# Performance work log

Measured on AMD Instinct MI355X. Metric: run time of the kernel, lower is better.

## Reference

```python
import jax, jax.numpy as jnp
import numpy as np

B, T, C = 4, 2048, 1024   # batch, seq_len, n_embd
H, D = 16, 64             # num heads, head dim (H*D == C)


def setup_inputs() -> dict:
    key = jax.random.key(0)
    ks = jax.random.split(key, 6)
    scale = 0.02
    x = jax.random.normal(ks[0], (B, T, C), dtype=jnp.float32)
    Wq = jax.random.normal(ks[1], (H, C, D), dtype=jnp.float32) * scale
    Wk = jax.random.normal(ks[2], (H, C, D), dtype=jnp.float32) * scale
    Wv = jax.random.normal(ks[3], (H, C, D), dtype=jnp.float32) * scale
    Wp = jax.random.normal(ks[4], (C, C), dtype=jnp.float32) * scale
    bp = jnp.zeros((C,), dtype=jnp.float32)
    return {"x": x, "Wq": Wq, "Wk": Wk, "Wv": Wv, "Wp": Wp, "bp": bp}


def reference(x, Wq, Wk, Wv, Wp, bp):
    # Batched per-head projections (equivalent to the per-head nn.Linear loop)
    q = jnp.einsum('btc,hcd->bhtd', x, Wq)
    k = jnp.einsum('btc,hcd->bhtd', x, Wk)
    v = jnp.einsum('btc,hcd->bhtd', x, Wv)
    # NOTE: original code scales by C**-0.5 where C = n_embd (not head dim)
    scores = jnp.einsum('bhtd,bhsd->bhts', q, k) * (C ** -0.5)
    causal = jnp.tril(jnp.ones((T, T), dtype=bool))  # [T, T]
    scores = jnp.where(causal, scores, -jnp.inf)
    att = jax.nn.softmax(scores, axis=-1)            # [B, H, T, T]
    out = jnp.einsum('bhts,bhsd->bhtd', att, v)      # [B, H, T, D]
    # concat heads (order matches torch.cat over head list) then output proj
    out = out.transpose(0, 2, 1, 3).reshape(B, T, H * D)
    return out @ Wp + bp
```

## Files before the change

kernel.cpp:

```cpp
#include <hip/hip_runtime.h>
#include <hip/hip_bf16.h>


#define B_ 4
#define T_ 2048
#define C_ 1024
#define H_ 16
#define D_ 64
#define M_ (B_*T_)

typedef unsigned short u16;
typedef unsigned short ushort8 __attribute__((ext_vector_type(8)));
typedef unsigned int uint4v __attribute__((ext_vector_type(4)));
typedef int int2v __attribute__((ext_vector_type(2)));
typedef __attribute__((ext_vector_type(8))) short bf16x8;
typedef __attribute__((ext_vector_type(4))) float f32x4;
typedef __attribute__((ext_vector_type(16))) float f32x16;

__device__ __forceinline__ u16 f2bf(float f) {
    __hip_bfloat16 h = __float2bfloat16(f);
    return *reinterpret_cast<u16*>(&h);
}

__device__ __forceinline__ unsigned pkt(float lo, float hi2) {
    return __builtin_amdgcn_perm(__float_as_uint(hi2), __float_as_uint(lo), 0x07060302u);
}

__device__ __forceinline__ void gload_lds16(const void* g, void* lds) {
    __builtin_amdgcn_global_load_lds((const __attribute__((address_space(1))) unsigned int*)g,
                                     (__attribute__((address_space(3))) unsigned int*)lds, 16, 0, 0);
}

__global__ __launch_bounds__(256) void cast_x(const float* __restrict__ in, u16* __restrict__ out) {
    int i = (blockIdx.x * 256 + threadIdx.x) * 8;
    float4 a = *reinterpret_cast<const float4*>(in + i);
    float4 b = *reinterpret_cast<const float4*>(in + i + 4);
    ushort8 o;
    o[0]=f2bf(a.x); o[1]=f2bf(a.y); o[2]=f2bf(a.z); o[3]=f2bf(a.w);
    o[4]=f2bf(b.x); o[5]=f2bf(b.y); o[6]=f2bf(b.z); o[7]=f2bf(b.w);
    *reinterpret_cast<ushort8*>(out + i) = o;
}

__device__ __forceinline__ void ttile64(const float* __restrict__ in, int ldin,
                                        u16* __restrict__ out, int ldout, float scale) {
    __shared__ float t[64][65];
    const int tid = threadIdx.x;
    {
        int c = tid & 63, rr = tid >> 6;
        #pragma unroll
        for (int i = 0; i < 16; ++i) {
            int r = i * 4 + rr;
            t[r][c] = in[(size_t)r * ldin + c];
        }
    }
    __syncthreads();
    {
        int r2 = tid & 63, cg = tid >> 6;
        #pragma unroll
        for (int i = 0; i < 16; ++i) {
            int cc = i * 4 + cg;
            out[(size_t)cc * ldout + r2] = f2bf(t[r2][cc] * scale);
        }
    }
}

__global__ __launch_bounds__(256) void tw_qkv(const float* __restrict__ Wq, const float* __restrict__ Wk,
                                              const float* __restrict__ Wv, u16* __restrict__ Wt) {
    const int z = blockIdx.y;
    const int which = z >> 4, h = z & 15;
    const float* W = (which == 0 ? Wq : which == 1 ? Wk : Wv) + (size_t)h * C_ * D_;
    const int r0 = blockIdx.x * 64;
    const float scale = (which == 0) ? 0.03125f * 1.4426950408889634f : 1.f;
    ttile64(W + (size_t)r0 * D_, D_, Wt + (size_t)(which * 16 + h) * 64 * C_ + r0, C_, scale);
}

__global__ __launch_bounds__(256) void tw_p(const float* __restrict__ Wp, u16* __restrict__ Wpt) {
    const int r0 = blockIdx.x * 64, c0 = blockIdx.y * 64;
    ttile64(Wp + (size_t)r0 * C_ + c0, C_, Wpt + (size_t)c0 * C_ + r0, C_, 1.f);
}

__global__ __launch_bounds__(256) void tv(const u16* __restrict__ v, u16* __restrict__ vT) {
    __shared__ u16 t[64][72];
    const int tid = threadIdx.x;
    const int t0 = blockIdx.x * 64, bh = blockIdx.y;
    const u16* src = v + ((size_t)bh * T_ + t0) * D_;
    #pragma unroll
    for (int it = 0; it < 2; ++it) {
        int idx = it * 256 + tid;
        int r = idx >> 3, c8 = (idx & 7) * 8;
        *reinterpret_cast<ushort8*>(&t[r][c8]) =
            *reinterpret_cast<const ushort8*>(src + (size_t)r * D_ + c8);
    }
    __syncthreads();
    #pragma unroll
    for (int it = 0; it < 2; ++it) {
        int idx = it * 256 + tid;
        int d = idx >> 3, c8 = (idx & 7) * 8;
        ushort8 w;
        #pragma unroll
        for (int i = 0; i < 8; ++i) w[i] = t[c8 + i][d];
        *reinterpret_cast<ushort8*>(vT + ((size_t)bh * D_ + d) * T_ + t0 + c8) = w;
    }
}

__device__ __forceinline__ void gemm128_core(const u16* __restrict__ A, const u16* __restrict__ Bt,
                                             int m0, int n0, int K,
                                             u16* Asm, u16* Bsm, f32x4 (&acc)[4][4]) {
    const int tid = threadIdx.x;
    const int wid = tid >> 6, lane = tid & 63;
    const int l16 = lane & 15, lq = lane >> 4;
    const int wm = wid >> 1, wn = wid & 1;
    const int srow = lane >> 2;
    const int scol = (lane & 3) * 8;

    for (int k0 = 0; k0 < K; k0 += 32) {
        __syncthreads();
        #pragma unroll
        for (int it = 0; it < 2; ++it) {
            int row = wid * 32 + it * 16 + srow;
            gload_lds16(A  + (size_t)(m0 + row) * K + k0 + scol, Asm + wid * 1024 + it * 512);
            gload_lds16(Bt + (size_t)(n0 + row) * K + k0 + scol, Bsm + wid * 1024 + it * 512);
        }
        __syncthreads();
        bf16x8 af[4], bfr[4];
        #pragma unroll
        for (int t = 0; t < 4; ++t) {
            af[t]  = *reinterpret_cast<const bf16x8*>(Asm + (wm * 64 + t * 16 + l16) * 32 + lq * 8);
            bfr[t] = *reinterpret_cast<const bf16x8*>(Bsm + (wn * 64 + t * 16 + l16) * 32 + lq * 8);
        }
        #pragma unroll
        for (int mt = 0; mt < 4; ++mt)
            #pragma unroll
            for (int nt = 0; nt < 4; ++nt)
                acc[mt][nt] = __builtin_amdgcn_mfma_f32_16x16x32_bf16(af[mt], bfr[nt], acc[mt][nt], 0, 0, 0);
    }
}

__global__ __launch_bounds__(256) void qkv_gemm(const u16* __restrict__ xb, const u16* __restrict__ Wt,
                                                u16* __restrict__ q, u16* __restrict__ k, u16* __restrict__ v) {
    __shared__ u16 Asm[128 * 32], Bsm[128 * 32];
    f32x4 acc[4][4];
    #pragma unroll
    for (int i = 0; i < 4; ++i)
        #pragma unroll
        for (int j = 0; j < 4; ++j) { acc[i][j][0]=0.f; acc[i][j][1]=0.f; acc[i][j][2]=0.f; acc[i][j][3]=0.f; }
    const int m0 = blockIdx.x * 128, n0 = blockIdx.y * 128;
    gemm128_core(xb, Wt, m0, n0, C_, Asm, Bsm, acc);

    const int tid = threadIdx.x, wid = tid >> 6, lane = tid & 63;
    const int l16 = lane & 15, lq = lane >> 4;
    const int wm = wid >> 1, wn = wid & 1;
    #pragma unroll
    for (int mt = 0; mt < 4; ++mt) {
        #pragma unroll
        for (int j = 0; j < 4; ++j) {
            int m = m0 + wm * 64 + mt * 16 + lq * 4 + j;
            int b = m >> 11, t = m & (T_ - 1);
            #pragma unroll
            for (int nt = 0; nt < 4; ++nt) {
                int n = n0 + wn * 64 + nt * 16 + l16;
                int which = n >> 10, h = (n >> 6) & 15, d = n & 63;
                u16* dst = (which == 0 ? q : which == 1 ? k : v);
                dst[((size_t)(b * H_ + h) * T_ + t) * D_ + d] = f2bf(acc[mt][nt][j]);
            }
        }
    }
}

__global__ __launch_bounds__(256) void out_gemm(const u16* __restrict__ ob, const u16* __restrict__ Wpt,
                                                const float* __restrict__ bp, float* __restrict__ out) {
    __shared__ u16 Asm[128 * 32], Bsm[128 * 32];
    f32x4 acc[4][4];
    #pragma unroll
    for (int i = 0; i < 4; ++i)
        #pragma unroll
        for (int j = 0; j < 4; ++j) { acc[i][j][0]=0.f; acc[i][j][1]=0.f; acc[i][j][2]=0.f; acc[i][j][3]=0.f; }
    const int m0 = blockIdx.x * 128, n0 = blockIdx.y * 128;
    gemm128_core(ob, Wpt, m0, n0, C_, Asm, Bsm, acc);

    const int tid = threadIdx.x, wid = tid >> 6, lane = tid & 63;
    const int l16 = lane & 15, lq = lane >> 4;
    const int wm = wid >> 1, wn = wid & 1;
    #pragma unroll
    for (int mt = 0; mt < 4; ++mt) {
        #pragma unroll
        for (int j = 0; j < 4; ++j) {
            int m = m0 + wm * 64 + mt * 16 + lq * 4 + j;
            #pragma unroll
            for (int nt = 0; nt < 4; ++nt) {
                int n = n0 + wn * 64 + nt * 16 + l16;
                out[(size_t)m * C_ + n] = acc[mt][nt][j] + bp[n];
            }
        }
    }
}

template<int CUR>
__device__ __forceinline__ void attn_tile(const char* const (&pf)[4], const bf16x8 (&qf)[4],
                                          const f32x16& z16, float& lrun,
                                          f32x16& oacc0, f32x16& oacc1,
                                          bool isdiag, int relq, int hi) {
    f32x16 st0, st1;
    __builtin_amdgcn_s_setprio(1);
    {
        bf16x8 ka0 = *reinterpret_cast<const bf16x8*>(pf[0] + CUR * 8192);
        bf16x8 ka1 = *reinterpret_cast<const bf16x8*>(pf[0] + CUR * 8192 + 4096);
        st0 = __builtin_amdgcn_mfma_f32_32x32x16_bf16(ka0, qf[0], z16, 0, 0, 0);
        st1 = __builtin_amdgcn_mfma_f32_32x32x16_bf16(ka1, qf[0], z16, 0, 0, 0);
    }
    #pragma unroll
    for (int kc = 1; kc < 4; ++kc) {
        bf16x8 ka0 = *reinterpret_cast<const bf16x8*>(pf[kc] + CUR * 8192);
        bf16x8 ka1 = *reinterpret_cast<const bf16x8*>(pf[kc] + CUR * 8192 + 4096);
        st0 = __builtin_amdgcn_mfma_f32_32x32x16_bf16(ka0, qf[kc], st0, 0, 0, 0);
        st1 = __builtin_amdgcn_mfma_f32_32x32x16_bf16(ka1, qf[kc], st1, 0, 0, 0);
    }
    __builtin_amdgcn_s_setprio(0);

    if (isdiag) {
        #pragma unroll
        for (int rr = 0; rr < 16; ++rr) {
            int sl = (rr & 3) + 8 * (rr >> 2) + 4 * hi;
            if (sl > relq)      st0[rr] = -INFINITY;
            if (sl + 32 > relq) st1[rr] = -INFINITY;
        }
    }

    float rsum = 0.f;
    #pragma unroll
    for (int rr = 0; rr < 16; ++rr) {
        st0[rr] = __builtin_amdgcn_exp2f(st0[rr]);
        st1[rr] = __builtin_amdgcn_exp2f(st1[rr]);
        rsum += st0[rr] + st1[rr];
    }
    rsum += __shfl_xor(rsum, 32);
    lrun += rsum;

    bf16x8 pa0, pa1, pa2, pa3;
#if __has_builtin(__builtin_amdgcn_permlane32_swap)
#define MK_PA(PA, SV, RB)                                                          \
    {                                                                              \
        int X0 = (int)pkt(SV[RB + 0], SV[RB + 1]);                                 \
        int X1 = (int)pkt(SV[RB + 2], SV[RB + 3]);                                 \
        int Y0 = (int)pkt(SV[RB + 4], SV[RB + 5]);                                 \
        int Y1 = (int)pkt(SV[RB + 6], SV[RB + 7]);                                 \
        int2v r0 = __builtin_amdgcn_permlane32_swap(X0, Y0, false, false);         \
        int2v r1 = __builtin_amdgcn_permlane32_swap(X1, Y1, false, false);         \
        uint4v w; w[0] = (unsigned)r0[0]; w[1] = (unsigned)r1[0];                  \
        w[2] = (unsigned)r0[1]; w[3] = (unsigned)r1[1];                            \
        PA = __builtin_bit_cast(bf16x8, w);                                        \
    }
#else
#define MK_PA(PA, SV, RB)                                                          \
    {                                                                              \
        unsigned X0 = pkt(SV[RB + 0], SV[RB + 1]);                                 \
        unsigned X1 = pkt(SV[RB + 2], SV[RB + 3]);                                 \
        unsigned Y0 = pkt(SV[RB + 4], SV[RB + 5]);                                 \
        unsigned sX0 = __shfl_xor(X0, 32), sY0 = __shfl_xor(Y0, 32);               \
        unsigned Y1 = pkt(SV[RB + 6], SV[RB + 7]);                                 \
        unsigned sX1 = __shfl_xor(X1, 32), sY1 = __shfl_xor(Y1, 32);               \
        uint4v w;                                                                  \
        w[0] = hi ? sY0 : X0; w[1] = hi ? sY1 : X1;                                \
        w[2] = hi ? Y0 : sX0; w[3] = hi ? Y1 : sX1;                                \
        PA = __builtin_bit_cast(bf16x8, w);                                        \
    }
#endif
    MK_PA(pa0, st0, 0); MK_PA(pa1, st0, 8); MK_PA(pa2, st1, 0); MK_PA(pa3, st1, 8);
#undef MK_PA

    __builtin_amdgcn_s_setprio(1);
#define PV_STEP(SCJ, PAV)                                                          \
    {                                                                              \
        bf16x8 va0 = *reinterpret_cast<const bf16x8*>(pf[SCJ] + 16384 + CUR * 8192);        \
        bf16x8 va1 = *reinterpret_cast<const bf16x8*>(pf[SCJ] + 16384 + CUR * 8192 + 4096); \
        oacc0 = __builtin_amdgcn_mfma_f32_32x32x16_bf16(va0, PAV, oacc0, 0, 0, 0); \
        oacc1 = __builtin_amdgcn_mfma_f32_32x32x16_bf16(va1, PAV, oacc1, 0, 0, 0); \
    }
    PV_STEP(0, pa0) PV_STEP(1, pa1) PV_STEP(2, pa2) PV_STEP(3, pa3)
#undef PV_STEP
    __builtin_amdgcn_s_setprio(0);
}

__global__ __launch_bounds__(256) void attn_mfma(const u16* __restrict__ q,
                                                 const u16* __restrict__ k,
                                                 const u16* __restrict__ vT,
                                                 u16* __restrict__ o) {
    __shared__ u16 smem[2][2][4096];

    const int tid  = threadIdx.x;
    const int wid  = tid >> 6;
    const int lane = tid & 63;
    const int l31  = lane & 31;
    const int hi   = lane >> 5;

    const int lin = blockIdx.x;
    const int r   = lin & 255;
    const int f   = lin >> 8;
    const int e   = r & 7;
    int qb, bh;
    if      (f == 0) { qb = e;      bh = (r >> 3);      }
    else if (f == 1) { qb = 15 - e; bh = (r >> 3);      }
    else if (f == 2) { qb = e + 8;  bh = (r >> 3) + 32; }
    else             { qb = 7 - e;  bh = (r >> 3) + 32; }

    const int q0 = qb * 128;
    const size_t base = (size_t)bh * T_ * D_;
    const u16* kp  = k  + base;
    const u16* vtp = vT + (size_t)bh * D_ * T_;
    const int qglob = q0 + wid * 32 + l31;

    bf16x8 qf[4];
    {
        const u16* qp = q + base + (size_t)qglob * D_;
        #pragma unroll
        for (int kc = 0; kc < 4; ++kc)
            qf[kc] = *reinterpret_cast<const bf16x8*>(qp + kc * 16 + hi * 8);
    }

    const int rw0 = wid * 8 + (lane >> 3);
    const int rw1 = rw0 + 32;
    const int cg  = (lane & 7) ^ (rw0 & 7);
    const u16* gK0 = kp + rw0 * D_ + cg * 8;
    const u16* gK1 = kp + rw1 * D_ + cg * 8;
    const u16* gV0 = vtp + (size_t)rw0 * T_ + cg * 8;
    const u16* gV1 = vtp + (size_t)rw1 * T_ + cg * 8;

    u16* sbase = &smem[0][0][0];
    u16* dK0 = sbase + wid * 512;
    u16* dK1 = sbase + 2048 + wid * 512;
    u16* dV0 = sbase + 8192 + wid * 512;
    u16* dV1 = sbase + 8192 + 2048 + wid * 512;

    const char* pf[4];
    #pragma unroll
    for (int j = 0; j < 4; ++j)
        pf[j] = reinterpret_cast<const char*>(sbase) + l31 * 128 + (((j * 2 + hi) ^ (l31 & 7)) << 4);

    float lrun = 0.f;
    f32x16 oacc0, oacc1, z16;
    #pragma unroll
    for (int rr = 0; rr < 16; ++rr) { oacc0[rr] = 0.f; oacc1[rr] = 0.f; z16[rr] = 0.f; }

    const int ntile  = 2 * qb + 2;
    const int diag_t = 2 * qb + (wid >> 1);
    const int relq   = 32 * (wid & 1) + l31;

#define STG(BUFOFF)                                                                \
    {                                                                              \
        gload_lds16(gK0, dK0 + (BUFOFF)); gload_lds16(gK1, dK1 + (BUFOFF));        \
        gload_lds16(gV0, dV0 + (BUFOFF)); gload_lds16(gV1, dV1 + (BUFOFF));        \
        gK0 += 64 * D_; gK1 += 64 * D_; gV0 += 64; gV1 += 64;                      \
    }

    STG(0);
    __syncthreads();

    for (int tt = 0; tt < ntile; tt += 2) {
        if (tt + 1 < ntile) STG(4096);
        if (tt <= diag_t)
            attn_tile<0>(pf, qf, z16, lrun, oacc0, oacc1, tt == diag_t, relq, hi);
        __syncthreads();
        if (tt + 2 < ntile) STG(0);
        if (tt + 1 <= diag_t)
            attn_tile<1>(pf, qf, z16, lrun, oacc0, oacc1, tt + 1 == diag_t, relq, hi);
        __syncthreads();
    }
#undef STG

    float linv = 1.f / lrun;
    float* ot = reinterpret_cast<float*>(sbase) + wid * 2048;
    #pragma unroll
    for (int rr = 0; rr < 16; ++rr) {
        int d0v = (rr & 3) + 8 * (rr >> 2) + 4 * hi;
        int d1v = d0v + 32;
        ot[l31 * 64 + (((d0v >> 2) ^ (l31 & 7)) << 2) + (d0v & 3)] = oacc0[rr] * linv;
        ot[l31 * 64 + (((d1v >> 2) ^ (l31 & 7)) << 2) + (d1v & 3)] = oacc1[rr] * linv;
    }

    const int b = bh >> 4, h = bh & 15;
    const int qrow = lane >> 1;
    const int d0 = (lane & 1) * 32;
    u16 tmp[32];
    #pragma unroll
    for (int i = 0; i < 8; ++i) {
        int g = ((d0 >> 2) + i) ^ (qrow & 7);
        float4 fv = *reinterpret_cast<const float4*>(&ot[qrow * 64 + (g << 2)]);
        tmp[i * 4 + 0] = f2bf(fv.x); tmp[i * 4 + 1] = f2bf(fv.y);
        tmp[i * 4 + 2] = f2bf(fv.z); tmp[i * 4 + 3] = f2bf(fv.w);
    }
    u16* orow = o + ((size_t)b * T_ + q0 + wid * 32 + qrow) * C_ + h * 64 + d0;
    #pragma unroll
    for (int j = 0; j < 4; ++j)
        *reinterpret_cast<ushort8*>(orow + j * 8) = *reinterpret_cast<ushort8*>(&tmp[j * 8]);
}

extern "C" void kernel_launch(void* const* d_in, const int* in_sizes, int n_in,
                              void* d_out, int out_size, void* d_ws, size_t ws_size,
                              hipStream_t stream) {
    const float* x  = (const float*)d_in[0];
    const float* Wq = (const float*)d_in[1];
    const float* Wk = (const float*)d_in[2];
    const float* Wv = (const float*)d_in[3];
    const float* Wp = (const float*)d_in[4];
    const float* bp = (const float*)d_in[5];
    float* out = (float*)d_out;

    const size_t E = (size_t)M_ * C_;
    u16* xb  = (u16*)d_ws;
    u16* qb  = xb  + E;
    u16* kb  = qb  + E;
    u16* vb  = kb  + E;
    u16* obf = vb  + E;
    u16* Wt  = obf + E;
    u16* Wpt = Wt  + (size_t)3072 * 1024;
    u16* vTb = xb;

    cast_x<<<(E / 2048), 256, 0, stream>>>(x, xb);
    tw_qkv<<<dim3(16, 48), 256, 0, stream>>>(Wq, Wk, Wv, Wt);
    tw_p<<<dim3(16, 16), 256, 0, stream>>>(Wp, Wpt);

    qkv_gemm<<<dim3(M_ / 128, 3072 / 128), 256, 0, stream>>>(xb, Wt, qb, kb, vb);

    tv<<<dim3(T_ / 64, B_ * H_), 256, 0, stream>>>(vb, vTb);

    attn_mfma<<<dim3(1024), 256, 0, stream>>>(qb, kb, vTb, obf);

    out_gemm<<<dim3(M_ / 128, C_ / 128), 256, 0, stream>>>(obf, Wpt, bp, out);
}
```

Measured before the change: 165.4 us.

## Use 512-thread blocks with triple-buffered swizzled GEMM and larger attention tiles

The GEMM core becomes a 256x128 tile using 512 threads, with a three-stage LDS ring buffer, swizzled LDS layout, explicit vmcnt waits and raw barriers, and setprio around the MFMA work. The attention kernel switches to 512-thread blocks, each covering 256 query rows, with single-load-per-thread K/V staging into a larger LDS buffer and a simpler block-to-work mapping. Together these aim to hide global-load latency and cut per-block overhead in both GEMMs and attention. The cost is more LDS per block, which can lower occupancy. The simpler attention mapping may also balance the causal workload less evenly than the previous paired scheme.

```diff
diff --git a/kernel.cpp b/kernel.cpp
--- a/kernel.cpp
+++ b/kernel.cpp
@@ -21,15 +21,14 @@
     __hip_bfloat16 h = __float2bfloat16(f);
     return *reinterpret_cast<u16*>(&h);
 }
-
 __device__ __forceinline__ unsigned pkt(float lo, float hi2) {
     return __builtin_amdgcn_perm(__float_as_uint(hi2), __float_as_uint(lo), 0x07060302u);
 }
-
 __device__ __forceinline__ void gload_lds16(const void* g, void* lds) {
     __builtin_amdgcn_global_load_lds((const __attribute__((address_space(1))) unsigned int*)g,
                                      (__attribute__((address_space(3))) unsigned int*)lds, 16, 0, 0);
 }
+__device__ __forceinline__ int swzf(int r) { return (r ^ (r >> 2)) & 3; }
 
 __global__ __launch_bounds__(256) void cast_x(const float* __restrict__ in, u16* __restrict__ out) {
     int i = (blockIdx.x * 256 + threadIdx.x) * 8;
@@ -103,62 +102,97 @@
     }
 }
 
-__device__ __forceinline__ void gemm128_core(const u16* __restrict__ A, const u16* __restrict__ Bt,
-                                             int m0, int n0, int K,
-                                             u16* Asm, u16* Bsm, f32x4 (&acc)[4][4]) {
+__device__ __forceinline__ void gemm_core(const u16* __restrict__ A, const u16* __restrict__ Bt,
+                                          int m0, int n0, u16* lds, f32x4 (&acc)[4][4]) {
     const int tid = threadIdx.x;
     const int wid = tid >> 6, lane = tid & 63;
     const int l16 = lane & 15, lq = lane >> 4;
-    const int wm = wid >> 1, wn = wid & 1;
-    const int srow = lane >> 2;
-    const int scol = (lane & 3) * 8;
-
-    for (int k0 = 0; k0 < K; k0 += 32) {
-        __syncthreads();
-        #pragma unroll
-        for (int it = 0; it < 2; ++it) {
-            int row = wid * 32 + it * 16 + srow;
-            gload_lds16(A  + (size_t)(m0 + row) * K + k0 + scol, Asm + wid * 1024 + it * 512);
-            gload_lds16(Bt + (size_t)(n0 + row) * K + k0 + scol, Bsm + wid * 1024 + it * 512);
-        }
-        __syncthreads();
-        bf16x8 af[4], bfr[4];
-        #pragma unroll
-        for (int t = 0; t < 4; ++t) {
-            af[t]  = *reinterpret_cast<const bf16x8*>(Asm + (wm * 64 + t * 16 + l16) * 32 + lq * 8);
-            bfr[t] = *reinterpret_cast<const bf16x8*>(Bsm + (wn * 64 + t * 16 + l16) * 32 + lq * 8);
-        }
-        #pragma unroll
-        for (int mt = 0; mt < 4; ++mt)
+    const int wr = wid >> 1, wc = wid & 1;
+
+    const int rA0 = tid >> 2, rA1 = 128 + (tid >> 2), rB = tid >> 2, gd = tid & 3;
+    const u16* sA0 = A  + (size_t)(m0 + rA0) * C_ + ((gd ^ swzf(rA0)) * 8);
+    const u16* sA1 = A  + (size_t)(m0 + rA1) * C_ + ((gd ^ swzf(rA1)) * 8);
+    const u16* sB0 = Bt + (size_t)(n0 + rB)  * C_ + ((gd ^ swzf(rB))  * 8);
+
+    const char* lb = reinterpret_cast<const char*>(lds);
+    const int gcol = ((lq ^ ((l16 ^ (l16 >> 2)) & 3)) & 3) * 16;
+    int aoff[4], boff[4];
+    #pragma unroll
+    for (int i = 0; i < 4; ++i) {
+        aoff[i] = (wr * 64 + i * 16 + l16) * 64 + gcol;
+        boff[i] = 16384 + (wc * 64 + i * 16 + l16) * 64 + gcol;
+    }
+
+#define STG3(BU16)                                                                  \
+    {                                                                               \
+        gload_lds16(sA0, lds + (BU16) + tid * 8);                                   \
+        gload_lds16(sA1, lds + (BU16) + 4096 + tid * 8);                            \
+        gload_lds16(sB0, lds + (BU16) + 8192 + tid * 8);                            \
+        sA0 += 32; sA1 += 32; sB0 += 32;                                            \
+    }
+
+    STG3(0);
+    STG3(12288);
+
+    #pragma unroll
+    for (int t = 0; t < 32; ++t) {
+        if (t + 2 < 32) {
+            STG3(((t + 2) % 3) * 12288);
+            asm volatile("s_waitcnt vmcnt(6)" ::: "memory");
+        } else if (t + 1 < 32) {
+            asm volatile("s_waitcnt vmcnt(3)" ::: "memory");
+        } else {
+            asm volatile("s_waitcnt vmcnt(0)" ::: "memory");
+        }
+        __builtin_amdgcn_sched_barrier(0);
+        __builtin_amdgcn_s_barrier();
+        __builtin_amdgcn_sched_barrier(0);
+
+        const char* lbuf = lb + (t % 3) * 24576;
+        __builtin_amdgcn_s_setprio(1);
+        bf16x8 bfr[4];
+        #pragma unroll
+        for (int nt = 0; nt < 4; ++nt)
+            bfr[nt] = *reinterpret_cast<const bf16x8*>(lbuf + boff[nt]);
+        #pragma unroll
+        for (int mt = 0; mt < 4; ++mt) {
+            bf16x8 af = *reinterpret_cast<const bf16x8*>(lbuf + aoff[mt]);
             #pragma unroll
             for (int nt = 0; nt < 4; ++nt)
-                acc[mt][nt] = __builtin_amdgcn_mfma_f32_16x16x32_bf16(af[mt], bfr[nt], acc[mt][nt], 0, 0, 0);
-    }
-}
-
-__global__ __launch_bounds__(256) void qkv_gemm(const u16* __restrict__ xb, const u16* __restrict__ Wt,
-                                                u16* __restrict__ q, u16* __restrict__ k, u16* __restrict__ v) {
-    __shared__ u16 Asm[128 * 32], Bsm[128 * 32];
+                acc[mt][nt] = __builtin_amdgcn_mfma_f32_16x16x32_bf16(af, bfr[nt], acc[mt][nt], 0, 0, 0);
+        }
+        __builtin_amdgcn_s_setprio(0);
+        __builtin_amdgcn_sched_barrier(0);
+        __builtin_amdgcn_s_barrier();
+        __builtin_amdgcn_sched_barrier(0);
+    }
+#undef STG3
+}
+
+__global__ __launch_bounds__(512, 4) void qkv_gemm(const u16* __restrict__ xb, const u16* __restrict__ Wt,
+                                                   u16* __restrict__ q, u16* __restrict__ k,
+                                                   u16* __restrict__ v) {
+    __shared__ u16 lds[3 * 12288];
     f32x4 acc[4][4];
     #pragma unroll
     for (int i = 0; i < 4; ++i)
         #pragma unroll
         for (int j = 0; j < 4; ++j) { acc[i][j][0]=0.f; acc[i][j][1]=0.f; acc[i][j][2]=0.f; acc[i][j][3]=0.f; }
-    const int m0 = blockIdx.x * 128, n0 = blockIdx.y * 128;
-    gemm128_core(xb, Wt, m0, n0, C_, Asm, Bsm, acc);
+    const int m0 = blockIdx.x * 256, n0 = blockIdx.y * 128;
+    gemm_core(xb, Wt, m0, n0, lds, acc);
 
     const int tid = threadIdx.x, wid = tid >> 6, lane = tid & 63;
     const int l16 = lane & 15, lq = lane >> 4;
-    const int wm = wid >> 1, wn = wid & 1;
+    const int wr = wid >> 1, wc = wid & 1;
     #pragma unroll
     for (int mt = 0; mt < 4; ++mt) {
         #pragma unroll
         for (int j = 0; j < 4; ++j) {
-            int m = m0 + wm * 64 + mt * 16 + lq * 4 + j;
+            int m = m0 + wr * 64 + mt * 16 + lq * 4 + j;
             int b = m >> 11, t = m & (T_ - 1);
             #pragma unroll
             for (int nt = 0; nt < 4; ++nt) {
-                int n = n0 + wn * 64 + nt * 16 + l16;
+                int n = n0 + wc * 64 + nt * 16 + l16;
                 int which = n >> 10, h = (n >> 6) & 15, d = n & 63;
                 u16* dst = (which == 0 ? q : which == 1 ? k : v);
                 dst[((size_t)(b * H_ + h) * T_ + t) * D_ + d] = f2bf(acc[mt][nt][j]);
@@ -167,28 +201,28 @@
     }
 }
 
-__global__ __launch_bounds__(256) void out_gemm(const u16* __restrict__ ob, const u16* __restrict__ Wpt,
-                                                const float* __restrict__ bp, float* __restrict__ out) {
-    __shared__ u16 Asm[128 * 32], Bsm[128 * 32];
+__global__ __launch_bounds__(512, 4) void out_gemm(const u16* __restrict__ ob, const u16* __restrict__ Wpt,
+                                                   const float* __restrict__ bp, float* __restrict__ out) {
+    __shared__ u16 lds[3 * 12288];
     f32x4 acc[4][4];
     #pragma unroll
     for (int i = 0; i < 4; ++i)
         #pragma unroll
         for (int j = 0; j < 4; ++j) { acc[i][j][0]=0.f; acc[i][j][1]=0.f; acc[i][j][2]=0.f; acc[i][j][3]=0.f; }
-    const int m0 = blockIdx.x * 128, n0 = blockIdx.y * 128;
-    gemm128_core(ob, Wpt, m0, n0, C_, Asm, Bsm, acc);
+    const int m0 = blockIdx.x * 256, n0 = blockIdx.y * 128;
+    gemm_core(ob, Wpt, m0, n0, lds, acc);
 
     const int tid = threadIdx.x, wid = tid >> 6, lane = tid & 63;
     const int l16 = lane & 15, lq = lane >> 4;
-    const int wm = wid >> 1, wn = wid & 1;
+    const int wr = wid >> 1, wc = wid & 1;
     #pragma unroll
     for (int mt = 0; mt < 4; ++mt) {
         #pragma unroll
         for (int j = 0; j < 4; ++j) {
-            int m = m0 + wm * 64 + mt * 16 + lq * 4 + j;
+            int m = m0 + wr * 64 + mt * 16 + lq * 4 + j;
             #pragma unroll
             for (int nt = 0; nt < 4; ++nt) {
-                int n = n0 + wn * 64 + nt * 16 + l16;
+                int n = n0 + wc * 64 + nt * 16 + l16;
                 out[(size_t)m * C_ + n] = acc[mt][nt][j] + bp[n];
             }
         }
@@ -203,15 +237,15 @@
     f32x16 st0, st1;
     __builtin_amdgcn_s_setprio(1);
     {
-        bf16x8 ka0 = *reinterpret_cast<const bf16x8*>(pf[0] + CUR * 8192);
-        bf16x8 ka1 = *reinterpret_cast<const bf16x8*>(pf[0] + CUR * 8192 + 4096);
+        bf16x8 ka0 = *reinterpret_cast<const bf16x8*>(pf[0] + CUR * 32768);
+        bf16x8 ka1 = *reinterpret_cast<const bf16x8*>(pf[0] + CUR * 32768 + 4096);
         st0 = __builtin_amdgcn_mfma_f32_32x32x16_bf16(ka0, qf[0], z16, 0, 0, 0);
         st1 = __builtin_amdgcn_mfma_f32_32x32x16_bf16(ka1, qf[0], z16, 0, 0, 0);
     }
     #pragma unroll
     for (int kc = 1; kc < 4; ++kc) {
-        bf16x8 ka0 = *reinterpret_cast<const bf16x8*>(pf[kc] + CUR * 8192);
-        bf16x8 ka1 = *reinterpret_cast<const bf16x8*>(pf[kc] + CUR * 8192 + 4096);
+        bf16x8 ka0 = *reinterpret_cast<const bf16x8*>(pf[kc] + CUR * 32768);
+        bf16x8 ka1 = *reinterpret_cast<const bf16x8*>(pf[kc] + CUR * 32768 + 4096);
         st0 = __builtin_amdgcn_mfma_f32_32x32x16_bf16(ka0, qf[kc], st0, 0, 0, 0);
         st1 = __builtin_amdgcn_mfma_f32_32x32x16_bf16(ka1, qf[kc], st1, 0, 0, 0);
     }
@@ -271,8 +305,8 @@
     __builtin_amdgcn_s_setprio(1);
 #define PV_STEP(SCJ, PAV)                                                          \
     {                                                                              \
-        bf16x8 va0 = *reinterpret_cast<const bf16x8*>(pf[SCJ] + 16384 + CUR * 8192);        \
-        bf16x8 va1 = *reinterpret_cast<const bf16x8*>(pf[SCJ] + 16384 + CUR * 8192 + 4096); \
+        bf16x8 va0 = *reinterpret_cast<const bf16x8*>(pf[SCJ] + CUR * 32768 + 16384);        \
+        bf16x8 va1 = *reinterpret_cast<const bf16x8*>(pf[SCJ] + CUR * 32768 + 16384 + 4096); \
         oacc0 = __builtin_amdgcn_mfma_f32_32x32x16_bf16(va0, PAV, oacc0, 0, 0, 0); \
         oacc1 = __builtin_amdgcn_mfma_f32_32x32x16_bf16(va1, PAV, oacc1, 0, 0, 0); \
     }
@@ -281,11 +315,11 @@
     __builtin_amdgcn_s_setprio(0);
 }
 
-__global__ __launch_bounds__(256) void attn_mfma(const u16* __restrict__ q,
-                                                 const u16* __restrict__ k,
-                                                 const u16* __restrict__ vT,
-                                                 u16* __restrict__ o) {
-    __shared__ u16 smem[2][2][4096];
+__global__ __launch_bounds__(512, 4) void attn_mfma(const u16* __restrict__ q,
+                                                    const u16* __restrict__ k,
+                                                    const u16* __restrict__ vT,
+                                                    u16* __restrict__ o) {
+    __shared__ u16 smem[32768];
 
     const int tid  = threadIdx.x;
     const int wid  = tid >> 6;
@@ -296,14 +330,11 @@
     const int lin = blockIdx.x;
     const int r   = lin & 255;
     const int f   = lin >> 8;
-    const int e   = r & 7;
-    int qb, bh;
-    if      (f == 0) { qb = e;      bh = (r >> 3);      }
-    else if (f == 1) { qb = 15 - e; bh = (r >> 3);      }
-    else if (f == 2) { qb = e + 8;  bh = (r >> 3) + 32; }
-    else             { qb = 7 - e;  bh = (r >> 3) + 32; }
-
-    const int q0 = qb * 128;
+    const int bh  = r & 63;
+    const int e   = r >> 6;
+    const int qb  = f ? (7 - e) : e;
+
+    const int q0 = qb * 256;
     const size_t base = (size_t)bh * T_ * D_;
     const u16* kp  = k  + base;
     const u16* vtp = vT + (size_t)bh * D_ * T_;
@@ -317,19 +348,14 @@
             qf[kc] = *reinterpret_cast<const bf16x8*>(qp + kc * 16 + hi * 8);
     }
 
-    const int rw0 = wid * 8 + (lane >> 3);
-    const int rw1 = rw0 + 32;
-    const int cg  = (lane & 7) ^ (rw0 & 7);
-    const u16* gK0 = kp + rw0 * D_ + cg * 8;
-    const u16* gK1 = kp + rw1 * D_ + cg * 8;
-    const u16* gV0 = vtp + (size_t)rw0 * T_ + cg * 8;
-    const u16* gV1 = vtp + (size_t)rw1 * T_ + cg * 8;
-
-    u16* sbase = &smem[0][0][0];
-    u16* dK0 = sbase + wid * 512;
-    u16* dK1 = sbase + 2048 + wid * 512;
-    u16* dV0 = sbase + 8192 + wid * 512;
-    u16* dV1 = sbase + 8192 + 2048 + wid * 512;
+    const int rw = tid >> 3;
+    const int cg = (tid & 7) ^ (rw & 7);
+    const u16* gK = kp  + (size_t)rw * D_ + cg * 8;
+    const u16* gV = vtp + (size_t)rw * T_ + cg * 8;
+
+    u16* sbase = &smem[0];
+    u16* dK = sbase + tid * 8;
+    u16* dV = sbase + 8192 + tid * 8;
 
     const char* pf[4];
     #pragma unroll
@@ -341,22 +367,21 @@
     #pragma unroll
     for (int rr = 0; rr < 16; ++rr) { oacc0[rr] = 0.f; oacc1[rr] = 0.f; z16[rr] = 0.f; }
 
-    const int ntile  = 2 * qb + 2;
-    const int diag_t = 2 * qb + (wid >> 1);
+    const int ntile  = 4 * qb + 4;
+    const int diag_t = 4 * qb + (wid >> 1);
     const int relq   = 32 * (wid & 1) + l31;
 
-#define STG(BUFOFF)                                                                \
+#define STG(BUFU16)                                                                \
     {                                                                              \
-        gload_lds16(gK0, dK0 + (BUFOFF)); gload_lds16(gK1, dK1 + (BUFOFF));        \
-        gload_lds16(gV0, dV0 + (BUFOFF)); gload_lds16(gV1, dV1 + (BUFOFF));        \
-        gK0 += 64 * D_; gK1 += 64 * D_; gV0 += 64; gV1 += 64;                      \
+        gload_lds16(gK, dK + (BUFU16)); gload_lds16(gV, dV + (BUFU16));            \
+        gK += 64 * D_; gV += 64;                                                   \
     }
 
     STG(0);
     __syncthreads();
 
     for (int tt = 0; tt < ntile; tt += 2) {
-        if (tt + 1 < ntile) STG(4096);
+        if (tt + 1 < ntile) STG(16384);
         if (tt <= diag_t)
             attn_tile<0>(pf, qf, z16, lrun, oacc0, oacc1, tt == diag_t, relq, hi);
         __syncthreads();
@@ -419,11 +444,11 @@
     tw_qkv<<<dim3(16, 48), 256, 0, stream>>>(Wq, Wk, Wv, Wt);
     tw_p<<<dim3(16, 16), 256, 0, stream>>>(Wp, Wpt);
 
-    qkv_gemm<<<dim3(M_ / 128, 3072 / 128), 256, 0, stream>>>(xb, Wt, qb, kb, vb);
+    qkv_gemm<<<dim3(M_ / 256, 3072 / 128), 512, 0, stream>>>(xb, Wt, qb, kb, vb);
 
     tv<<<dim3(T_ / 64, B_ * H_), 256, 0, stream>>>(vb, vTb);
 
-    attn_mfma<<<dim3(1024), 256, 0, stream>>>(qb, kb, vTb, obf);
-
-    out_gemm<<<dim3(M_ / 128, C_ / 128), 256, 0, stream>>>(obf, Wpt, bp, out);
-}
+    attn_mfma<<<dim3(512), 512, 0, stream>>>(qb, kb, vTb, obf);
+
+    out_gemm<<<dim3(M_ / 256, C_ / 128), 512, 0, stream>>>(obf, Wpt, bp, out);
+}
```

Result: faster. 149.8 us (-9.4%).
